# Performance work log

Measured on AMD Instinct MI355X. Metric: run time of the kernel, lower is better.

The kernel has to match this reference:

```python
import jax, jax.numpy as jnp
import numpy as np

SCALE = 2

def setup_inputs() -> dict:
    key = jax.random.key(0)
    ks = jax.random.split(key, 8)
    b, c, h, w = 4, 64, 128, 128
    C = c * SCALE * SCALE  # 256
    Cq = C // 8            # 32
    return {
        "x": jax.random.normal(ks[0], (b, c, h, w), dtype=jnp.float32),
        "wq": jax.random.normal(ks[1], (Cq, C), dtype=jnp.float32) * 0.05,
        "bq": jax.random.normal(ks[2], (Cq,), dtype=jnp.float32) * 0.05,
        "wk": jax.random.normal(ks[3], (Cq, C), dtype=jnp.float32) * 0.05,
        "bk": jax.random.normal(ks[4], (Cq,), dtype=jnp.float32) * 0.05,
        "wv": jax.random.normal(ks[5], (C, C), dtype=jnp.float32) * 0.05,
        "bv": jax.random.normal(ks[6], (C,), dtype=jnp.float32) * 0.05,
        "gamma": jax.random.normal(ks[7], (1,), dtype=jnp.float32) * 0.1,
    }

def _space_to_depth(x, s):
    # faithful to the torch permute/view chain: (b,c,h,w) -> (b, c*s*s, h//s, w//s)
    b, c, h, w = x.shape
    xp = jnp.transpose(x, (0, 3, 2, 1)).reshape(b, w, h // s, c * s)
    xp = jnp.transpose(xp, (0, 2, 1, 3)).reshape(b, h // s, w // s, c * s * s)
    return jnp.transpose(xp, (0, 3, 1, 2))

def _depth_to_space(y, s):
    # inverse rearrange: (b, C, H, W) -> (b, C//(s*s), H*s, W*s)
    B, C, H, W = y.shape
    yp = jnp.transpose(y, (0, 2, 3, 1)).reshape(B, H, W * s, C // s)
    yp = jnp.transpose(yp, (0, 2, 1, 3)).reshape(B, W * s, H * s, C // (s * s))
    return jnp.transpose(yp, (0, 3, 2, 1))

def reference(x, wq, bq, wk, bk, wv, bv, gamma):
    s = SCALE
    xp = _space_to_depth(x, s)            # (B, C, H, W)
    B, C, H, W = xp.shape
    N = H * W
    # 1x1 convs as channel matmuls
    q = jnp.einsum('bchw,oc->bohw', xp, wq) + bq[None, :, None, None]
    k = jnp.einsum('bchw,oc->bohw', xp, wk) + bk[None, :, None, None]
    v = jnp.einsum('bchw,oc->bohw', xp, wv) + bv[None, :, None, None]
    q = q.reshape(B, -1, N)               # (B, Cq, N)
    k = k.reshape(B, -1, N)               # (B, Cq, N)
    v = v.reshape(B, C, N)                # (B, C, N)
    energy = jnp.einsum('bcn,bcm->bnm', q, k)          # (B, N, N), no scaling (faithful)
    attention = jax.nn.softmax(energy, axis=-1)
    out = jnp.einsum('bcm,bnm->bcn', v, attention)     # value @ attention^T
    out = out.reshape(B, C, H, W)
    out = gamma * out + xp
    return _depth_to_space(out, s)        # back to (b, c, h, w)
```

## Files before the change

### kernel.cpp

```cpp
#include <hip/hip_runtime.h>

typedef __bf16 bf16_t;
typedef __bf16 bf16x2 __attribute__((ext_vector_type(2)));
typedef __bf16 bf16x8 __attribute__((ext_vector_type(8)));
typedef float  f32x4  __attribute__((ext_vector_type(4)));
typedef float  f32x16 __attribute__((ext_vector_type(16)));
typedef unsigned u32x4 __attribute__((ext_vector_type(4)));

#define HIN 128
#define WIN 128
#define LOG2E 1.4426950408889634f

__device__ __forceinline__ unsigned pk(float a, float b) {
    bf16x2 v; v[0] = (bf16_t)a; v[1] = (bf16_t)b;
    return __builtin_bit_cast(unsigned, v);
}

__device__ __forceinline__ void glds16(const bf16_t* g, bf16_t* l) {
    __builtin_amdgcn_global_load_lds(
        (const __attribute__((address_space(1))) unsigned int*)g,
        (__attribute__((address_space(3))) unsigned int*)l, 16, 0, 0);
}

__device__ __forceinline__ int vperm16(int p) {
    return (p & 3) | (((p >> 3) & 1) << 2) | (((p >> 2) & 1) << 3);
}

__global__ __launch_bounds__(1024) void prep_kernel(
    const float* __restrict__ wq, const float* __restrict__ bq,
    const float* __restrict__ wk, const float* __restrict__ bk,
    const float* __restrict__ wv, const float* __restrict__ bv,
    bf16_t* __restrict__ Wb, float* __restrict__ Ball)
{
    int idx = blockIdx.x * 1024 + threadIdx.x;
    int row = idx >> 8, c = idx & 255;
    const float* src = row < 32 ? wq + (size_t)row * 256
                     : row < 64 ? wk + (size_t)(row - 32) * 256
                                : wv + (size_t)(row - 64) * 256;
    Wb[idx] = (bf16_t)src[c];
    if (idx < 320)
        Ball[idx] = idx < 32 ? bq[idx] : idx < 64 ? bk[idx - 32] : bv[idx - 64];
}

__global__ __launch_bounds__(256) void proj_kernel(
    const float* __restrict__ x, const bf16_t* __restrict__ Wb,
    const float* __restrict__ Ball,
    bf16_t* __restrict__ Qg, bf16_t* __restrict__ Kg, bf16_t* __restrict__ Vg)
{
    __shared__ __attribute__((aligned(16))) bf16_t Xs[32 * 256];
    __shared__ bf16_t Ls[320 * 34];
    const int blk  = blockIdx.x;
    const int half = blk & 1;
    const int h2   = (blk >> 1) & 63;
    const int b    = blk >> 7;
    const int tid  = threadIdx.x;

    const float* xb = x + ((size_t)b << 20);
    for (int s = 0; s < 8; ++s) {
        int v   = tid + (s << 8);
        int cin = v >> 5;
        int hb  = (v >> 4) & 1;
        int w4l = v & 15;
        const float4 xv = *(const float4*)(xb + ((size_t)cin * HIN + (2*h2 + hb)) * WIN
                                           + ((half * 16 + w4l) << 2));
        float vals[4] = {xv.x, xv.y, xv.z, xv.w};
        #pragma unroll
        for (int j = 0; j < 4; ++j) {
            int nl = ((w4l << 2) + j) >> 1;
            int c  = ((j & 1) << 7) + (hb << 6) + cin;
            int chunk = c >> 3;
            int phys  = chunk ^ (nl & 7);
            Xs[(nl << 8) + (phys << 3) + (c & 7)] = (bf16_t)vals[j];
        }
    }
    __syncthreads();

    const int ln = tid & 63;
    const int w  = tid >> 6;
    const int l  = ln & 15;
    const int q  = ln >> 4;

    int row_o[5];
    #pragma unroll
    for (int i = 0; i < 5; ++i) row_o[i] = (w * 5 + i) * 16 + l;

    f32x4 acc[5][2];
    #pragma unroll
    for (int i = 0; i < 5; ++i) {
        float bias = Ball[row_o[i]];
        #pragma unroll
        for (int nt = 0; nt < 2; ++nt) {
            acc[i][nt][0] = bias; acc[i][nt][1] = bias;
            acc[i][nt][2] = bias; acc[i][nt][3] = bias;
        }
    }

    for (int ks = 0; ks < 8; ++ks) {
        bf16x8 a[2];
        #pragma unroll
        for (int nt = 0; nt < 2; ++nt) {
            int phys = ((ks << 2) + q) ^ (l & 7);
            a[nt] = *(const bf16x8*)&Xs[((nt * 16 + l) << 8) + (phys << 3)];
        }
        #pragma unroll
        for (int i = 0; i < 5; ++i) {
            const bf16x8 bw = *(const bf16x8*)(Wb + (size_t)row_o[i] * 256 + (ks << 5) + (q << 3));
            #pragma unroll
            for (int nt = 0; nt < 2; ++nt)
                acc[i][nt] = __builtin_amdgcn_mfma_f32_16x16x32_bf16(a[nt], bw, acc[i][nt], 0, 0, 0);
        }
    }

    #pragma unroll
    for (int i = 0; i < 5; ++i)
        #pragma unroll
        for (int nt = 0; nt < 2; ++nt)
            #pragma unroll
            for (int reg = 0; reg < 4; ++reg)
                Ls[row_o[i] * 34 + nt * 16 + q * 4 + reg] = (bf16_t)acc[i][nt][reg];
    __syncthreads();

    const int nbase = h2 * 64 + half * 32;
    {
        int task = tid >> 7;
        int v    = tid & 127;
        int n    = v >> 2, part = v & 3;
        bf16x8 pkv;
        #pragma unroll
        for (int j = 0; j < 8; ++j)
            pkv[j] = Ls[(task * 32 + part * 8 + j) * 34 + n];
        bf16_t* dst = task ? Kg : Qg;
        *(bf16x8*)(dst + (((size_t)(b * 4096 + nbase + n)) << 5) + part * 8) = pkv;
    }
    for (int pass = 0; pass < 4; ++pass) {
        int u = pass * 256 + tid;
        int c = u >> 2, part = u & 3;
        bf16x8 pv;
        #pragma unroll
        for (int j = 0; j < 8; ++j) {
            int p  = part * 8 + j;
            int nl = (p & 16) | vperm16(p & 15);
            pv[j] = Ls[(64 + c) * 34 + nl];
        }
        *(bf16x8*)(Vg + (((size_t)(b * 256 + c)) << 12) + nbase + part * 8) = pv;
    }
}

__global__ __launch_bounds__(256, 2) void attn_kernel(
    const bf16_t* __restrict__ Qg, const bf16_t* __restrict__ Kg,
    const bf16_t* __restrict__ Vg, bf16_t* __restrict__ Pp,
    float* __restrict__ Lp, int T, int S)
{
    __shared__ __attribute__((aligned(16))) bf16_t Vs[2][16384];
    __shared__ __attribute__((aligned(16))) bf16_t Ksh[2][2048];

    const int blk = blockIdx.x;
    int b, qt, s;
    if (S == 4) {
        int xcd = blk & 7;
        b = xcd >> 1;
        int g = blk >> 3;
        qt = g >> 1;
        s  = (xcd & 1) * 2 + (g & 1);
    } else {
        b = blk & 3;
        int rest = blk >> 2;
        qt = rest & 31;
        s  = rest >> 5;
    }
    const int n0 = qt * 128;

    const int tid  = threadIdx.x;
    const int wv   = tid >> 6;
    const int lane = tid & 63;
    const int i    = lane & 31;
    const int h    = lane >> 5;

    const bf16_t* Qb = Qg + ((size_t)b << 17);
    const bf16_t* Kb = Kg + ((size_t)b << 17);
    const bf16_t* Vb = Vg + ((size_t)(b * 256) << 12);

    bf16x8 Qf[2];
    #pragma unroll
    for (int dc = 0; dc < 2; ++dc)
        Qf[dc] = *(const bf16x8*)(Qb + (size_t)(n0 + wv * 32 + i) * 32 + dc * 16 + h * 8);

    f32x16 acc[8];
    #pragma unroll
    for (int cb = 0; cb < 8; ++cb)
        #pragma unroll
        for (int r = 0; r < 16; ++r) acc[cb][r] = 0.f;
    float lrow = 0.f;
    const f32x16 z16 = acc[0];

    auto stage = [&](int buf, int m0) {
        #pragma unroll
        for (int r = 0; r < 8; ++r) {
            int ub = (r * 4 + wv) * 64;
            int u  = ub + lane;
            int c  = u >> 3;
            int ks = (u & 7) ^ (c & 7);
            glds16(Vb + ((size_t)c << 12) + m0 + ks * 8, &Vs[buf][ub * 8]);
        }
        {
            int u2 = wv * 64 + lane;
            int m  = u2 >> 2;
            int kk = (u2 & 3) ^ (m & 3);
            glds16(Kb + (size_t)(m0 + m) * 32 + kk * 8, &Ksh[buf][(wv * 64) * 8]);
        }
    };

    stage(0, s * T * 64);

    for (int t = 0; t < T; ++t) {
        __asm__ volatile("s_waitcnt vmcnt(0)" ::: "memory");
        __asm__ volatile("s_barrier" ::: "memory");

        if (t + 1 < T)
            stage((t + 1) & 1, (s * T + t + 1) * 64);

        const bf16_t* Vt = Vs[t & 1];
        const bf16_t* Kt = Ksh[t & 1];

        bf16x8 Kf[2][2];
        #pragma unroll
        for (int mb = 0; mb < 2; ++mb)
            #pragma unroll
            for (int dc = 0; dc < 2; ++dc) {
                int m = mb * 32 + i;
                int cc = (dc * 2 + h) ^ (i & 3);
                Kf[mb][dc] = *(const bf16x8*)&Kt[m * 32 + cc * 8];
            }

        f32x16 sT[2];
        #pragma unroll
        for (int mb = 0; mb < 2; ++mb) {
            sT[mb] = __builtin_amdgcn_mfma_f32_32x32x16_bf16(Kf[mb][0], Qf[0], z16, 0, 0, 0);
            sT[mb] = __builtin_amdgcn_mfma_f32_32x32x16_bf16(Kf[mb][1], Qf[1], sT[mb], 0, 0, 0);
        }

        float psum = 0.f;
        #pragma unroll
        for (int mb = 0; mb < 2; ++mb)
            #pragma unroll
            for (int r = 0; r < 16; ++r) {
                float p = __builtin_amdgcn_exp2f(
                    __builtin_fmaf(sT[mb][r], LOG2E, -28.0f));
                sT[mb][r] = p;
                psum += p;
            }
        lrow += psum;

        bf16x8 Pf[4];
        #pragma unroll
        for (int mc = 0; mc < 4; ++mc) {
            int mb = mc >> 1, base = (mc & 1) * 8;
            u32x4 u;
            u[0] = pk(sT[mb][base + 0], sT[mb][base + 1]);
            u[1] = pk(sT[mb][base + 2], sT[mb][base + 3]);
            u[2] = pk(sT[mb][base + 4], sT[mb][base + 5]);
            u[3] = pk(sT[mb][base + 6], sT[mb][base + 7]);
            Pf[mc] = __builtin_bit_cast(bf16x8, u);
        }

        #pragma unroll
        for (int mc = 0; mc < 4; ++mc) {
            #pragma unroll
            for (int cb = 0; cb < 8; ++cb) {
                int c = cb * 32 + i;
                int phys = (2 * mc + h) ^ (c & 7);
                const bf16x8 Vf = *(const bf16x8*)&Vt[c * 64 + phys * 8];
                acc[cb] = __builtin_amdgcn_mfma_f32_32x32x16_bf16(Vf, Pf[mc], acc[cb], 0, 0, 0);
            }
        }
    }

    lrow += __shfl_xor(lrow, 32);

    const size_t pb = ((size_t)(s * 4 + b)) << 20;
    const int n = n0 + wv * 32 + i;
    bf16_t* prow = Pp + pb + ((size_t)n << 8);
    #pragma unroll
    for (int cb = 0; cb < 8; ++cb) {
        #pragma unroll
        for (int g = 0; g < 4; ++g) {
            int c_base = cb * 32 + g * 8 + h * 4;
            uint2 dv;
            dv.x = pk(acc[cb][g * 4 + 0], acc[cb][g * 4 + 1]);
            dv.y = pk(acc[cb][g * 4 + 2], acc[cb][g * 4 + 3]);
            *(uint2*)(prow + c_base) = dv;
        }
    }
    if (h == 0)
        Lp[((size_t)(s * 4 + b) << 12) + n] = lrow;
}

__global__ __launch_bounds__(256) void epi_kernel(
    const bf16_t* __restrict__ Pp, const float* __restrict__ Lp,
    const float* __restrict__ x, const float* __restrict__ gamma,
    float* __restrict__ out, int S)
{
    __shared__ __attribute__((aligned(16))) float Os[32 * 256];
    __shared__ float winv[32];
    const int blk  = blockIdx.x;
    const int half = blk & 1;
    const int h2   = (blk >> 1) & 63;
    const int b    = blk >> 7;
    const int tid  = threadIdx.x;
    const int nbase = h2 * 64 + half * 32;

    if (tid < 32) {
        int n = nbase + tid;
        float L = 0.f;
        for (int s = 0; s < S; ++s)
            L += Lp[((size_t)(s * 4 + b) << 12) + n];
        winv[tid] = 1.0f / L;
    }
    __syncthreads();

    for (int it = 0; it < 4; ++it) {
        int v  = tid + (it << 8);
        int i  = v >> 5;
        int ch = v & 31;
        int n  = nbase + i;
        float fo[8] = {0.f,0.f,0.f,0.f,0.f,0.f,0.f,0.f};
        for (int s = 0; s < S; ++s) {
            bf16x8 pv = *(const bf16x8*)(Pp + ((size_t)(s * 4 + b) << 20)
                                            + ((size_t)n << 8) + (ch << 3));
            #pragma unroll
            for (int e8 = 0; e8 < 8; ++e8) fo[e8] += (float)pv[e8];
        }
        float wn = winv[i];
        #pragma unroll
        for (int e8 = 0; e8 < 8; ++e8) fo[e8] *= wn;
        #pragma unroll
        for (int hh = 0; hh < 2; ++hh) {
            int f = (ch << 1) + hh;
            int phys = f ^ (i & 15) ^ ((f >> 3) & 4);
            *(float4*)&Os[(i << 8) + (phys << 2)] =
                float4{fo[hh*4+0], fo[hh*4+1], fo[hh*4+2], fo[hh*4+3]};
        }
    }
    __syncthreads();

    const float g = gamma[0];
    const float* xb = x + ((size_t)b << 20);
    float* ob       = out + ((size_t)b << 20);
    for (int it = 0; it < 8; ++it) {
        int uu  = tid + (it << 8);
        int e4  = uu >> 7;
        int h1b = (uu >> 6) & 1;
        int w1l = uu & 63;
        int i   = w1l >> 1;
        int f   = ((w1l & 1) << 5) | (h1b << 4) | e4;
        int phys = f ^ (i & 15) ^ ((f >> 3) & 4);
        float4 ov = *(const float4*)&Os[(i << 8) + (phys << 2)];
        float vals[4] = {ov.x, ov.y, ov.z, ov.w};
        int w1 = (half << 6) + w1l;
        #pragma unroll
        for (int k = 0; k < 4; ++k) {
            int e  = (e4 << 2) + k;
            int xi = (e * HIN + (2 * h2 + h1b)) * WIN + w1;
            ob[xi] = g * vals[k] + xb[xi];
        }
    }
}

extern "C" void kernel_launch(void* const* d_in, const int* in_sizes, int n_in,
                              void* d_out, int out_size, void* d_ws, size_t ws_size,
                              hipStream_t stream) {
    const float* x  = (const float*)d_in[0];
    const float* wq = (const float*)d_in[1];
    const float* bq = (const float*)d_in[2];
    const float* wk = (const float*)d_in[3];
    const float* bk = (const float*)d_in[4];
    const float* wv = (const float*)d_in[5];
    const float* bv = (const float*)d_in[6];
    const float* gm = (const float*)d_in[7];
    float* out = (float*)d_out;

    char* ws = (char*)d_ws;
    bf16_t* Qg = (bf16_t*)(ws);
    bf16_t* Kg = (bf16_t*)(ws + (1u << 20));
    bf16_t* Vg = (bf16_t*)(ws + (2u << 20));
    const size_t pp_off = (size_t)10 << 20;

    int S = 1;
    if (pp_off + 2 * (((size_t)8 << 20) + ((size_t)128 << 10)) <= ws_size) S = 2;
    if (pp_off + 4 * (((size_t)8 << 20) + ((size_t)128 << 10)) <= ws_size) S = 4;
    bf16_t* Pp = (bf16_t*)(ws + pp_off);
    float*  Lp = (float*)(ws + pp_off + (size_t)S * ((size_t)8 << 20));
    int T = 64 / S;

    bf16_t* Wb   = (bf16_t*)(ws + pp_off);
    float*  Ball = (float*)(ws + pp_off + (320 * 256 * 2));

    hipLaunchKernelGGL(prep_kernel, dim3(80), dim3(1024), 0, stream,
                       wq, bq, wk, bk, wv, bv, Wb, Ball);
    hipLaunchKernelGGL(proj_kernel, dim3(512), dim3(256), 0, stream,
                       x, Wb, Ball, Qg, Kg, Vg);
    hipLaunchKernelGGL(attn_kernel, dim3(128 * S), dim3(256), 0, stream,
                       Qg, Kg, Vg, Pp, Lp, T, S);
    hipLaunchKernelGGL(epi_kernel, dim3(512), dim3(256), 0, stream,
                       Pp, Lp, x, gm, out, S);
}
```

Measured before the change: 149.4 us.

## Fold weight prep into projection; split attention channels across waves, single-buffer LDS

Removes the separate weight-prep kernel launch: the projection kernel now reads the fp32 weights and biases directly and converts them to bf16 in registers. The attention kernel now handles 64 query rows per block instead of 128. Its four waves are split two ways by query half and two ways by channel half, which halves the accumulator registers per wave. LDS drops from double to single buffering with an extra barrier per tile, so occupancy can rise to 3 blocks per CU. The trade-off is that prefetch no longer overlaps compute, and each K/V tile is loaded twice as often across the grid.

```diff
diff --git a/kernel.cpp b/kernel.cpp
--- a/kernel.cpp
+++ b/kernel.cpp
@@ -26,25 +26,11 @@
     return (p & 3) | (((p >> 3) & 1) << 2) | (((p >> 2) & 1) << 3);
 }
 
-__global__ __launch_bounds__(1024) void prep_kernel(
+__global__ __launch_bounds__(256) void proj_kernel(
+    const float* __restrict__ x,
     const float* __restrict__ wq, const float* __restrict__ bq,
     const float* __restrict__ wk, const float* __restrict__ bk,
     const float* __restrict__ wv, const float* __restrict__ bv,
-    bf16_t* __restrict__ Wb, float* __restrict__ Ball)
-{
-    int idx = blockIdx.x * 1024 + threadIdx.x;
-    int row = idx >> 8, c = idx & 255;
-    const float* src = row < 32 ? wq + (size_t)row * 256
-                     : row < 64 ? wk + (size_t)(row - 32) * 256
-                                : wv + (size_t)(row - 64) * 256;
-    Wb[idx] = (bf16_t)src[c];
-    if (idx < 320)
-        Ball[idx] = idx < 32 ? bq[idx] : idx < 64 ? bk[idx - 32] : bv[idx - 64];
-}
-
-__global__ __launch_bounds__(256) void proj_kernel(
-    const float* __restrict__ x, const bf16_t* __restrict__ Wb,
-    const float* __restrict__ Ball,
     bf16_t* __restrict__ Qg, bf16_t* __restrict__ Kg, bf16_t* __restrict__ Vg)
 {
     __shared__ __attribute__((aligned(16))) bf16_t Xs[32 * 256];
@@ -80,14 +66,18 @@
     const int l  = ln & 15;
     const int q  = ln >> 4;
 
+    const float* wrow[5];
     int row_o[5];
-    #pragma unroll
-    for (int i = 0; i < 5; ++i) row_o[i] = (w * 5 + i) * 16 + l;
-
     f32x4 acc[5][2];
     #pragma unroll
     for (int i = 0; i < 5; ++i) {
-        float bias = Ball[row_o[i]];
+        int ot = w * 5 + i;
+        int o  = ot * 16 + l;
+        row_o[i] = o;
+        float bias;
+        if (ot < 2)      { wrow[i] = wq + (size_t)o * 256;        bias = bq[o]; }
+        else if (ot < 4) { wrow[i] = wk + (size_t)(o - 32) * 256; bias = bk[o - 32]; }
+        else             { wrow[i] = wv + (size_t)(o - 64) * 256; bias = bv[o - 64]; }
         #pragma unroll
         for (int nt = 0; nt < 2; ++nt) {
             acc[i][nt][0] = bias; acc[i][nt][1] = bias;
@@ -104,7 +94,11 @@
         }
         #pragma unroll
         for (int i = 0; i < 5; ++i) {
-            const bf16x8 bw = *(const bf16x8*)(Wb + (size_t)row_o[i] * 256 + (ks << 5) + (q << 3));
+            const float* wp = wrow[i] + (ks << 5) + (q << 3);
+            float4 w0 = *(const float4*)wp;
+            float4 w1 = *(const float4*)(wp + 4);
+            bf16x8 bw = { (bf16_t)w0.x, (bf16_t)w0.y, (bf16_t)w0.z, (bf16_t)w0.w,
+                          (bf16_t)w1.x, (bf16_t)w1.y, (bf16_t)w1.z, (bf16_t)w1.w };
             #pragma unroll
             for (int nt = 0; nt < 2; ++nt)
                 acc[i][nt] = __builtin_amdgcn_mfma_f32_16x16x32_bf16(a[nt], bw, acc[i][nt], 0, 0, 0);
@@ -146,13 +140,13 @@
     }
 }
 
-__global__ __launch_bounds__(256, 2) void attn_kernel(
+__global__ __launch_bounds__(256, 3) void attn_kernel(
     const bf16_t* __restrict__ Qg, const bf16_t* __restrict__ Kg,
     const bf16_t* __restrict__ Vg, bf16_t* __restrict__ Pp,
     float* __restrict__ Lp, int T, int S)
 {
-    __shared__ __attribute__((aligned(16))) bf16_t Vs[2][16384];
-    __shared__ __attribute__((aligned(16))) bf16_t Ksh[2][2048];
+    __shared__ __attribute__((aligned(16))) bf16_t Vs[16384];
+    __shared__ __attribute__((aligned(16))) bf16_t Ksh[2048];
 
     const int blk = blockIdx.x;
     int b, qt, s;
@@ -165,13 +159,15 @@
     } else {
         b = blk & 3;
         int rest = blk >> 2;
-        qt = rest & 31;
-        s  = rest >> 5;
-    }
-    const int n0 = qt * 128;
+        qt = rest & 63;
+        s  = rest >> 6;
+    }
+    const int n0 = qt * 64;
 
     const int tid  = threadIdx.x;
     const int wv   = tid >> 6;
+    const int qf   = wv & 1;
+    const int ch   = wv >> 1;
     const int lane = tid & 63;
     const int i    = lane & 31;
     const int h    = lane >> 5;
@@ -183,45 +179,39 @@
     bf16x8 Qf[2];
     #pragma unroll
     for (int dc = 0; dc < 2; ++dc)
-        Qf[dc] = *(const bf16x8*)(Qb + (size_t)(n0 + wv * 32 + i) * 32 + dc * 16 + h * 8);
-
-    f32x16 acc[8];
-    #pragma unroll
-    for (int cb = 0; cb < 8; ++cb)
+        Qf[dc] = *(const bf16x8*)(Qb + (size_t)(n0 + qf * 32 + i) * 32 + dc * 16 + h * 8);
+
+    f32x16 acc[4];
+    #pragma unroll
+    for (int cb = 0; cb < 4; ++cb)
         #pragma unroll
         for (int r = 0; r < 16; ++r) acc[cb][r] = 0.f;
     float lrow = 0.f;
     const f32x16 z16 = acc[0];
 
-    auto stage = [&](int buf, int m0) {
+    auto stage = [&](int m0) {
         #pragma unroll
         for (int r = 0; r < 8; ++r) {
             int ub = (r * 4 + wv) * 64;
             int u  = ub + lane;
             int c  = u >> 3;
             int ks = (u & 7) ^ (c & 7);
-            glds16(Vb + ((size_t)c << 12) + m0 + ks * 8, &Vs[buf][ub * 8]);
+            glds16(Vb + ((size_t)c << 12) + m0 + ks * 8, &Vs[ub * 8]);
         }
         {
             int u2 = wv * 64 + lane;
             int m  = u2 >> 2;
             int kk = (u2 & 3) ^ (m & 3);
-            glds16(Kb + (size_t)(m0 + m) * 32 + kk * 8, &Ksh[buf][(wv * 64) * 8]);
+            glds16(Kb + (size_t)(m0 + m) * 32 + kk * 8, &Ksh[(wv * 64) * 8]);
         }
     };
 
-    stage(0, s * T * 64);
+    stage(s * T * 64);
 
     for (int t = 0; t < T; ++t) {
         __asm__ volatile("s_waitcnt vmcnt(0)" ::: "memory");
         __asm__ volatile("s_barrier" ::: "memory");
 
-        if (t + 1 < T)
-            stage((t + 1) & 1, (s * T + t + 1) * 64);
-
-        const bf16_t* Vt = Vs[t & 1];
-        const bf16_t* Kt = Ksh[t & 1];
-
         bf16x8 Kf[2][2];
         #pragma unroll
         for (int mb = 0; mb < 2; ++mb)
@@ -229,7 +219,7 @@
             for (int dc = 0; dc < 2; ++dc) {
                 int m = mb * 32 + i;
                 int cc = (dc * 2 + h) ^ (i & 3);
-                Kf[mb][dc] = *(const bf16x8*)&Kt[m * 32 + cc * 8];
+                Kf[mb][dc] = *(const bf16x8*)&Ksh[m * 32 + cc * 8];
             }
 
         f32x16 sT[2];
@@ -266,32 +256,37 @@
         #pragma unroll
         for (int mc = 0; mc < 4; ++mc) {
             #pragma unroll
-            for (int cb = 0; cb < 8; ++cb) {
-                int c = cb * 32 + i;
+            for (int cb = 0; cb < 4; ++cb) {
+                int c = ch * 128 + cb * 32 + i;
                 int phys = (2 * mc + h) ^ (c & 7);
-                const bf16x8 Vf = *(const bf16x8*)&Vt[c * 64 + phys * 8];
+                const bf16x8 Vf = *(const bf16x8*)&Vs[c * 64 + phys * 8];
                 acc[cb] = __builtin_amdgcn_mfma_f32_32x32x16_bf16(Vf, Pf[mc], acc[cb], 0, 0, 0);
             }
         }
+
+        __asm__ volatile("s_waitcnt lgkmcnt(0)" ::: "memory");
+        __asm__ volatile("s_barrier" ::: "memory");
+        if (t + 1 < T)
+            stage((s * T + t + 1) * 64);
     }
 
     lrow += __shfl_xor(lrow, 32);
 
     const size_t pb = ((size_t)(s * 4 + b)) << 20;
-    const int n = n0 + wv * 32 + i;
+    const int n = n0 + qf * 32 + i;
     bf16_t* prow = Pp + pb + ((size_t)n << 8);
     #pragma unroll
-    for (int cb = 0; cb < 8; ++cb) {
+    for (int cb = 0; cb < 4; ++cb) {
         #pragma unroll
         for (int g = 0; g < 4; ++g) {
-            int c_base = cb * 32 + g * 8 + h * 4;
+            int c_base = ch * 128 + cb * 32 + g * 8 + h * 4;
             uint2 dv;
             dv.x = pk(acc[cb][g * 4 + 0], acc[cb][g * 4 + 1]);
             dv.y = pk(acc[cb][g * 4 + 2], acc[cb][g * 4 + 3]);
             *(uint2*)(prow + c_base) = dv;
         }
     }
-    if (h == 0)
+    if (h == 0 && ch == 0)
         Lp[((size_t)(s * 4 + b) << 12) + n] = lrow;
 }
 
@@ -392,14 +387,9 @@
     float*  Lp = (float*)(ws + pp_off + (size_t)S * ((size_t)8 << 20));
     int T = 64 / S;
 
-    bf16_t* Wb   = (bf16_t*)(ws + pp_off);
-    float*  Ball = (float*)(ws + pp_off + (320 * 256 * 2));
-
-    hipLaunchKernelGGL(prep_kernel, dim3(80), dim3(1024), 0, stream,
-                       wq, bq, wk, bk, wv, bv, Wb, Ball);
     hipLaunchKernelGGL(proj_kernel, dim3(512), dim3(256), 0, stream,
-                       x, Wb, Ball, Qg, Kg, Vg);
-    hipLaunchKernelGGL(attn_kernel, dim3(128 * S), dim3(256), 0, stream,
+                       x, wq, bq, wk, bk, wv, bv, Qg, Kg, Vg);
+    hipLaunchKernelGGL(attn_kernel, dim3(256 * S), dim3(256), 0, stream,
                        Qg, Kg, Vg, Pp, Lp, T, S);
     hipLaunchKernelGGL(epi_kernel, dim3(512), dim3(256), 0, stream,
                        Pp, Lp, x, gm, out, S);
```

Result: slower. 173.4 us (+16.1%).

## Drop prep kernel, fuse weight conversion into projection, retile attention waves

Applied to the files above, without the earlier changes.

The separate weight-conversion kernel is removed. The projection kernel now reads fp32 weights directly and converts them to bf16 in registers. It also writes Q/K/V straight from the MFMA accumulators instead of staging them through an LDS transpose buffer. The attention kernel is retiled so each wave handles two 32-query groups over half of the channels, which reuses each V fragment load across two MFMAs. In exchange, the attention kernel now runs twice as many QK^T MFMAs per block and holds more registers, and each projection block re-reads and re-converts the fp32 weights.

```diff
diff --git a/kernel.cpp b/kernel.cpp
--- a/kernel.cpp
+++ b/kernel.cpp
@@ -22,33 +22,22 @@
         (__attribute__((address_space(3))) unsigned int*)l, 16, 0, 0);
 }
 
-__device__ __forceinline__ int vperm16(int p) {
-    return (p & 3) | (((p >> 3) & 1) << 2) | (((p >> 2) & 1) << 3);
-}
-
-__global__ __launch_bounds__(1024) void prep_kernel(
+__device__ __forceinline__ bf16x8 cvt8(const float* p) {
+    float4 w0 = *(const float4*)p;
+    float4 w1 = *(const float4*)(p + 4);
+    bf16x8 r = { (bf16_t)w0.x, (bf16_t)w0.y, (bf16_t)w0.z, (bf16_t)w0.w,
+                 (bf16_t)w1.x, (bf16_t)w1.y, (bf16_t)w1.z, (bf16_t)w1.w };
+    return r;
+}
+
+__global__ __launch_bounds__(256) void proj_kernel(
+    const float* __restrict__ x,
     const float* __restrict__ wq, const float* __restrict__ bq,
     const float* __restrict__ wk, const float* __restrict__ bk,
     const float* __restrict__ wv, const float* __restrict__ bv,
-    bf16_t* __restrict__ Wb, float* __restrict__ Ball)
-{
-    int idx = blockIdx.x * 1024 + threadIdx.x;
-    int row = idx >> 8, c = idx & 255;
-    const float* src = row < 32 ? wq + (size_t)row * 256
-                     : row < 64 ? wk + (size_t)(row - 32) * 256
-                                : wv + (size_t)(row - 64) * 256;
-    Wb[idx] = (bf16_t)src[c];
-    if (idx < 320)
-        Ball[idx] = idx < 32 ? bq[idx] : idx < 64 ? bk[idx - 32] : bv[idx - 64];
-}
-
-__global__ __launch_bounds__(256) void proj_kernel(
-    const float* __restrict__ x, const bf16_t* __restrict__ Wb,
-    const float* __restrict__ Ball,
     bf16_t* __restrict__ Qg, bf16_t* __restrict__ Kg, bf16_t* __restrict__ Vg)
 {
     __shared__ __attribute__((aligned(16))) bf16_t Xs[32 * 256];
-    __shared__ bf16_t Ls[320 * 34];
     const int blk  = blockIdx.x;
     const int half = blk & 1;
     const int h2   = (blk >> 1) & 63;
@@ -79,70 +68,67 @@
     const int w  = tid >> 6;
     const int l  = ln & 15;
     const int q  = ln >> 4;
-
-    int row_o[5];
-    #pragma unroll
-    for (int i = 0; i < 5; ++i) row_o[i] = (w * 5 + i) * 16 + l;
-
-    f32x4 acc[5][2];
-    #pragma unroll
-    for (int i = 0; i < 5; ++i) {
-        float bias = Ball[row_o[i]];
-        #pragma unroll
-        for (int nt = 0; nt < 2; ++nt) {
-            acc[i][nt][0] = bias; acc[i][nt][1] = bias;
-            acc[i][nt][2] = bias; acc[i][nt][3] = bias;
-        }
-    }
-
-    for (int ks = 0; ks < 8; ++ks) {
-        bf16x8 a[2];
-        #pragma unroll
-        for (int nt = 0; nt < 2; ++nt) {
-            int phys = ((ks << 2) + q) ^ (l & 7);
-            a[nt] = *(const bf16x8*)&Xs[((nt * 16 + l) << 8) + (phys << 3)];
-        }
-        #pragma unroll
-        for (int i = 0; i < 5; ++i) {
-            const bf16x8 bw = *(const bf16x8*)(Wb + (size_t)row_o[i] * 256 + (ks << 5) + (q << 3));
-            #pragma unroll
-            for (int nt = 0; nt < 2; ++nt)
-                acc[i][nt] = __builtin_amdgcn_mfma_f32_16x16x32_bf16(a[nt], bw, acc[i][nt], 0, 0, 0);
-        }
-    }
-
-    #pragma unroll
-    for (int i = 0; i < 5; ++i)
-        #pragma unroll
-        for (int nt = 0; nt < 2; ++nt)
-            #pragma unroll
-            for (int reg = 0; reg < 4; ++reg)
-                Ls[row_o[i] * 34 + nt * 16 + q * 4 + reg] = (bf16_t)acc[i][nt][reg];
-    __syncthreads();
-
     const int nbase = h2 * 64 + half * 32;
-    {
-        int task = tid >> 7;
-        int v    = tid & 127;
-        int n    = v >> 2, part = v & 3;
-        bf16x8 pkv;
-        #pragma unroll
-        for (int j = 0; j < 8; ++j)
-            pkv[j] = Ls[(task * 32 + part * 8 + j) * 34 + n];
-        bf16_t* dst = task ? Kg : Qg;
-        *(bf16x8*)(dst + (((size_t)(b * 4096 + nbase + n)) << 5) + part * 8) = pkv;
-    }
-    for (int pass = 0; pass < 4; ++pass) {
-        int u = pass * 256 + tid;
-        int c = u >> 2, part = u & 3;
-        bf16x8 pv;
-        #pragma unroll
-        for (int j = 0; j < 8; ++j) {
-            int p  = part * 8 + j;
-            int nl = (p & 16) | vperm16(p & 15);
-            pv[j] = Ls[(64 + c) * 34 + nl];
-        }
-        *(bf16x8*)(Vg + (((size_t)(b * 256 + c)) << 12) + nbase + part * 8) = pv;
+
+    for (int it = 0; it < 5; ++it) {
+        int ot = w * 5 + it;
+        if (ot < 4) {
+            const float* W  = (ot < 2) ? wq : wk;
+            const float* Bp = (ot < 2) ? bq : bk;
+            int o0 = (ot & 1) * 16;
+            float4 b4 = *(const float4*)&Bp[o0 + q * 4];
+            f32x4 acc[2];
+            #pragma unroll
+            for (int nt = 0; nt < 2; ++nt) {
+                acc[nt][0] = b4.x; acc[nt][1] = b4.y;
+                acc[nt][2] = b4.z; acc[nt][3] = b4.w;
+            }
+            for (int ks = 0; ks < 8; ++ks) {
+                bf16x8 aw = cvt8(W + (size_t)(o0 + l) * 256 + (ks << 5) + (q << 3));
+                #pragma unroll
+                for (int nt = 0; nt < 2; ++nt) {
+                    int phys = ((ks << 2) + q) ^ (l & 7);
+                    const bf16x8 bx = *(const bf16x8*)&Xs[((nt * 16 + l) << 8) + (phys << 3)];
+                    acc[nt] = __builtin_amdgcn_mfma_f32_16x16x32_bf16(aw, bx, acc[nt], 0, 0, 0);
+                }
+            }
+            bf16_t* dst = (ot < 2) ? Qg : Kg;
+            #pragma unroll
+            for (int nt = 0; nt < 2; ++nt) {
+                int n = nbase + nt * 16 + l;
+                uint2 dv;
+                dv.x = pk(acc[nt][0], acc[nt][1]);
+                dv.y = pk(acc[nt][2], acc[nt][3]);
+                *(uint2*)(dst + (((size_t)(b * 4096 + n)) << 5) + o0 + q * 4) = dv;
+            }
+        } else {
+            int c0 = (ot - 4) * 16;
+            float bias = bv[c0 + l];
+            f32x4 acc[2];
+            #pragma unroll
+            for (int nt = 0; nt < 2; ++nt) {
+                acc[nt][0] = bias; acc[nt][1] = bias;
+                acc[nt][2] = bias; acc[nt][3] = bias;
+            }
+            for (int ks = 0; ks < 8; ++ks) {
+                bf16x8 bw = cvt8(wv + (size_t)(c0 + l) * 256 + (ks << 5) + (q << 3));
+                #pragma unroll
+                for (int nt = 0; nt < 2; ++nt) {
+                    int phys = ((ks << 2) + q) ^ (l & 7);
+                    const bf16x8 ax = *(const bf16x8*)&Xs[((nt * 16 + l) << 8) + (phys << 3)];
+                    acc[nt] = __builtin_amdgcn_mfma_f32_16x16x32_bf16(ax, bw, acc[nt], 0, 0, 0);
+                }
+            }
+            int mloc = 4 * (q >> 1) + 8 * (q & 1);
+            #pragma unroll
+            for (int nt = 0; nt < 2; ++nt) {
+                uint2 dv;
+                dv.x = pk(acc[nt][0], acc[nt][1]);
+                dv.y = pk(acc[nt][2], acc[nt][3]);
+                *(uint2*)(Vg + (((size_t)(b * 256 + c0 + l)) << 12)
+                             + nbase + nt * 16 + mloc) = dv;
+            }
+        }
     }
 }
 
@@ -172,6 +158,8 @@
 
     const int tid  = threadIdx.x;
     const int wv   = tid >> 6;
+    const int p    = wv & 1;
+    const int ch   = wv >> 1;
     const int lane = tid & 63;
     const int i    = lane & 31;
     const int h    = lane >> 5;
@@ -180,18 +168,23 @@
     const bf16_t* Kb = Kg + ((size_t)b << 17);
     const bf16_t* Vb = Vg + ((size_t)(b * 256) << 12);
 
-    bf16x8 Qf[2];
+    bf16x8 Qf[2][2];
     #pragma unroll
-    for (int dc = 0; dc < 2; ++dc)
-        Qf[dc] = *(const bf16x8*)(Qb + (size_t)(n0 + wv * 32 + i) * 32 + dc * 16 + h * 8);
-
-    f32x16 acc[8];
+    for (int qg = 0; qg < 2; ++qg)
+        #pragma unroll
+        for (int dc = 0; dc < 2; ++dc)
+            Qf[qg][dc] = *(const bf16x8*)(Qb + (size_t)(n0 + p * 64 + qg * 32 + i) * 32
+                                             + dc * 16 + h * 8);
+
+    f32x16 acc[2][4];
     #pragma unroll
-    for (int cb = 0; cb < 8; ++cb)
-        #pragma unroll
-        for (int r = 0; r < 16; ++r) acc[cb][r] = 0.f;
-    float lrow = 0.f;
-    const f32x16 z16 = acc[0];
+    for (int qg = 0; qg < 2; ++qg)
+        #pragma unroll
+        for (int cb = 0; cb < 4; ++cb)
+            #pragma unroll
+            for (int r = 0; r < 16; ++r) acc[qg][cb][r] = 0.f;
+    float lrow[2] = {0.f, 0.f};
+    const f32x16 z16 = acc[0][0];
 
     auto stage = [&](int buf, int m0) {
         #pragma unroll
@@ -232,67 +225,78 @@
                 Kf[mb][dc] = *(const bf16x8*)&Kt[m * 32 + cc * 8];
             }
 
-        f32x16 sT[2];
-        #pragma unroll
-        for (int mb = 0; mb < 2; ++mb) {
-            sT[mb] = __builtin_amdgcn_mfma_f32_32x32x16_bf16(Kf[mb][0], Qf[0], z16, 0, 0, 0);
-            sT[mb] = __builtin_amdgcn_mfma_f32_32x32x16_bf16(Kf[mb][1], Qf[1], sT[mb], 0, 0, 0);
-        }
-
-        float psum = 0.f;
-        #pragma unroll
-        for (int mb = 0; mb < 2; ++mb)
-            #pragma unroll
-            for (int r = 0; r < 16; ++r) {
-                float p = __builtin_amdgcn_exp2f(
-                    __builtin_fmaf(sT[mb][r], LOG2E, -28.0f));
-                sT[mb][r] = p;
-                psum += p;
-            }
-        lrow += psum;
-
-        bf16x8 Pf[4];
+        f32x16 sT[2][2];
+        #pragma unroll
+        for (int qg = 0; qg < 2; ++qg)
+            #pragma unroll
+            for (int mb = 0; mb < 2; ++mb) {
+                sT[qg][mb] = __builtin_amdgcn_mfma_f32_32x32x16_bf16(Kf[mb][0], Qf[qg][0], z16, 0, 0, 0);
+                sT[qg][mb] = __builtin_amdgcn_mfma_f32_32x32x16_bf16(Kf[mb][1], Qf[qg][1], sT[qg][mb], 0, 0, 0);
+            }
+
+        #pragma unroll
+        for (int qg = 0; qg < 2; ++qg) {
+            float psum = 0.f;
+            #pragma unroll
+            for (int mb = 0; mb < 2; ++mb)
+                #pragma unroll
+                for (int r = 0; r < 16; ++r) {
+                    float pv = __builtin_amdgcn_exp2f(
+                        __builtin_fmaf(sT[qg][mb][r], LOG2E, -28.0f));
+                    sT[qg][mb][r] = pv;
+                    psum += pv;
+                }
+            lrow[qg] += psum;
+        }
+
         #pragma unroll
         for (int mc = 0; mc < 4; ++mc) {
-            int mb = mc >> 1, base = (mc & 1) * 8;
-            u32x4 u;
-            u[0] = pk(sT[mb][base + 0], sT[mb][base + 1]);
-            u[1] = pk(sT[mb][base + 2], sT[mb][base + 3]);
-            u[2] = pk(sT[mb][base + 4], sT[mb][base + 5]);
-            u[3] = pk(sT[mb][base + 6], sT[mb][base + 7]);
-            Pf[mc] = __builtin_bit_cast(bf16x8, u);
-        }
-
-        #pragma unroll
-        for (int mc = 0; mc < 4; ++mc) {
-            #pragma unroll
-            for (int cb = 0; cb < 8; ++cb) {
-                int c = cb * 32 + i;
+            bf16x8 Pf[2];
+            #pragma unroll
+            for (int qg = 0; qg < 2; ++qg) {
+                int mb = mc >> 1, base = (mc & 1) * 8;
+                u32x4 u;
+                u[0] = pk(sT[qg][mb][base + 0], sT[qg][mb][base + 1]);
+                u[1] = pk(sT[qg][mb][base + 2], sT[qg][mb][base + 3]);
+                u[2] = pk(sT[qg][mb][base + 4], sT[qg][mb][base + 5]);
+                u[3] = pk(sT[qg][mb][base + 6], sT[qg][mb][base + 7]);
+                Pf[qg] = __builtin_bit_cast(bf16x8, u);
+            }
+            #pragma unroll
+            for (int cb = 0; cb < 4; ++cb) {
+                int c = ch * 128 + cb * 32 + i;
                 int phys = (2 * mc + h) ^ (c & 7);
                 const bf16x8 Vf = *(const bf16x8*)&Vt[c * 64 + phys * 8];
-                acc[cb] = __builtin_amdgcn_mfma_f32_32x32x16_bf16(Vf, Pf[mc], acc[cb], 0, 0, 0);
-            }
-        }
-    }
-
-    lrow += __shfl_xor(lrow, 32);
+                #pragma unroll
+                for (int qg = 0; qg < 2; ++qg)
+                    acc[qg][cb] = __builtin_amdgcn_mfma_f32_32x32x16_bf16(Vf, Pf[qg], acc[qg][cb], 0, 0, 0);
+            }
+        }
+    }
+
+    #pragma unroll
+    for (int qg = 0; qg < 2; ++qg)
+        lrow[qg] += __shfl_xor(lrow[qg], 32);
 
     const size_t pb = ((size_t)(s * 4 + b)) << 20;
-    const int n = n0 + wv * 32 + i;
-    bf16_t* prow = Pp + pb + ((size_t)n << 8);
     #pragma unroll
-    for (int cb = 0; cb < 8; ++cb) {
-        #pragma unroll
-        for (int g = 0; g < 4; ++g) {
-            int c_base = cb * 32 + g * 8 + h * 4;
-            uint2 dv;
-            dv.x = pk(acc[cb][g * 4 + 0], acc[cb][g * 4 + 1]);
-            dv.y = pk(acc[cb][g * 4 + 2], acc[cb][g * 4 + 3]);
-            *(uint2*)(prow + c_base) = dv;
-        }
-    }
-    if (h == 0)
-        Lp[((size_t)(s * 4 + b) << 12) + n] = lrow;
+    for (int qg = 0; qg < 2; ++qg) {
+        const int n = n0 + p * 64 + qg * 32 + i;
+        bf16_t* prow = Pp + pb + ((size_t)n << 8);
+        #pragma unroll
+        for (int cb = 0; cb < 4; ++cb) {
+            #pragma unroll
+            for (int g = 0; g < 4; ++g) {
+                int c_base = ch * 128 + cb * 32 + g * 8 + h * 4;
+                uint2 dv;
+                dv.x = pk(acc[qg][cb][g * 4 + 0], acc[qg][cb][g * 4 + 1]);
+                dv.y = pk(acc[qg][cb][g * 4 + 2], acc[qg][cb][g * 4 + 3]);
+                *(uint2*)(prow + c_base) = dv;
+            }
+        }
+        if (h == 0 && ch == 0)
+            Lp[((size_t)(s * 4 + b) << 12) + n] = lrow[qg];
+    }
 }
 
 __global__ __launch_bounds__(256) void epi_kernel(
@@ -392,13 +396,8 @@
     float*  Lp = (float*)(ws + pp_off + (size_t)S * ((size_t)8 << 20));
     int T = 64 / S;
 
-    bf16_t* Wb   = (bf16_t*)(ws + pp_off);
-    float*  Ball = (float*)(ws + pp_off + (320 * 256 * 2));
-
-    hipLaunchKernelGGL(prep_kernel, dim3(80), dim3(1024), 0, stream,
-                       wq, bq, wk, bk, wv, bv, Wb, Ball);
     hipLaunchKernelGGL(proj_kernel, dim3(512), dim3(256), 0, stream,
-                       x, Wb, Ball, Qg, Kg, Vg);
+                       x, wq, bq, wk, bk, wv, bv, Qg, Kg, Vg);
     hipLaunchKernelGGL(attn_kernel, dim3(128 * S), dim3(256), 0, stream,
                        Qg, Kg, Vg, Pp, Lp, T, S);
     hipLaunchKernelGGL(epi_kernel, dim3(512), dim3(256), 0, stream,
```

Measured after the change: 190.9 us. 27.8% more time.
